# Kernel tuning notes

Measured on AMD Instinct MI355X. Metric: run time of the kernel, lower is better.

Reference implementation:

```python
import jax, jax.numpy as jnp
import numpy as np

DIM = 4096
N_HEADS = 32
N_KV_HEADS = 8
HEAD_DIM = DIM // N_HEADS  # 128
N_REP = N_HEADS // N_KV_HEADS  # 4
HIDDEN = 14336  # 4*dim -> 2/3 -> *1.3 -> round up to multiple of 256
EPS = 1e-6
BSZ, SEQLEN, CACHE_LEN = 1, 2048, 4096
ROPE_THETA = 500000.0


def setup_inputs() -> dict:
    key = jax.random.key(0)
    ks = jax.random.split(key, 16)
    s = 0.02
    x = jax.random.normal(ks[0], (BSZ, SEQLEN, DIM), jnp.float32)
    cache_k = jax.random.normal(ks[1], (BSZ, CACHE_LEN, N_KV_HEADS, HEAD_DIM), jnp.float32)
    cache_v = jax.random.normal(ks[2], (BSZ, CACHE_LEN, N_KV_HEADS, HEAD_DIM), jnp.float32)
    # causal mask over rolling cache: query i may attend to cache slot j <= (CACHE_LEN - SEQLEN) + i
    qi = jnp.arange(SEQLEN)[:, None]
    kj = jnp.arange(CACHE_LEN)[None, :]
    mask = jnp.where(kj <= (CACHE_LEN - SEQLEN) + qi, 0.0, -1e9).astype(jnp.float32)[None, None]
    # rotary freqs (cos/sin pairs) for the new seqlen positions (start of window here)
    inv = 1.0 / (ROPE_THETA ** (jnp.arange(0, HEAD_DIM, 2, dtype=jnp.float32) / HEAD_DIM))
    t = jnp.arange(SEQLEN, dtype=jnp.float32)
    ang = t[:, None] * inv[None, :]  # [S, HEAD_DIM//2]
    freqs_cis = jnp.stack([jnp.cos(ang), jnp.sin(ang)], axis=-1)  # [S, HD//2, 2]
    # params (stored as (in, out))
    wq = jax.random.normal(ks[3], (DIM, N_HEADS * HEAD_DIM), jnp.float32) * s
    wk = jax.random.normal(ks[4], (DIM, N_KV_HEADS * HEAD_DIM), jnp.float32) * s
    wv = jax.random.normal(ks[5], (DIM, N_KV_HEADS * HEAD_DIM), jnp.float32) * s
    wo = jax.random.normal(ks[6], (N_HEADS * HEAD_DIM, DIM), jnp.float32) * s
    w1 = jax.random.normal(ks[7], (DIM, HIDDEN), jnp.float32) * s
    w2 = jax.random.normal(ks[8], (HIDDEN, DIM), jnp.float32) * s
    w3 = jax.random.normal(ks[9], (DIM, HIDDEN), jnp.float32) * s
    attn_norm_w = jnp.ones((DIM,), jnp.float32)
    ffn_norm_w = jnp.ones((DIM,), jnp.float32)
    return dict(x=x, mask=mask, freqs_cis=freqs_cis, cache_k=cache_k, cache_v=cache_v,
                wq=wq, wk=wk, wv=wv, wo=wo, w1=w1, w2=w2, w3=w3,
                attn_norm_w=attn_norm_w, ffn_norm_w=ffn_norm_w)


def rmsnorm(x, w, eps=EPS):
    return x * jax.lax.rsqrt(jnp.mean(x * x, axis=-1, keepdims=True) + eps) * w


def apply_rope(xq, xk, freqs_cis):
    # xq: [B,S,Hq,D], xk: [B,S,Hkv,D]; freqs_cis: [S, D//2, 2]
    cos = freqs_cis[None, :, None, :, 0]  # [1,S,1,D//2]
    sin = freqs_cis[None, :, None, :, 1]
    def rot(t):
        tp = t.reshape(*t.shape[:-1], -1, 2)
        t0, t1 = tp[..., 0], tp[..., 1]
        o0 = t0 * cos - t1 * sin
        o1 = t0 * sin + t1 * cos
        return jnp.stack([o0, o1], axis=-1).reshape(t.shape)
    return rot(xq), rot(xk)


def reference(x, mask, freqs_cis, cache_k, cache_v, wq, wk, wv, wo, w1, w2, w3, attn_norm_w, ffn_norm_w):
    bsz, seqlen, _ = x.shape
    # --- attention norm ---
    xn = rmsnorm(x, attn_norm_w)
    # --- qkv ---
    xq = (xn @ wq).reshape(bsz, seqlen, N_HEADS, HEAD_DIM)
    xk = (xn @ wk).reshape(bsz, seqlen, N_KV_HEADS, HEAD_DIM)
    xv = (xn @ wv).reshape(bsz, seqlen, N_KV_HEADS, HEAD_DIM)
    xq, xk = apply_rope(xq, xk, freqs_cis)
    # --- rolling KV cache ---
    cache_k = jnp.concatenate([cache_k[:, seqlen:], xk], axis=1)  # [B,CL,Hkv,D]
    cache_v = jnp.concatenate([cache_v[:, seqlen:], xv], axis=1)
    keys = jnp.repeat(cache_k[:bsz], N_REP, axis=2)    # [B,CL,Hq,D]
    values = jnp.repeat(cache_v[:bsz], N_REP, axis=2)
    # --- attention ---
    scores = jnp.einsum('bqhd,bkhd->bhqk', xq, keys) / jnp.sqrt(jnp.float32(HEAD_DIM))
    scores = jax.nn.softmax(scores + mask, axis=-1)
    attn = jnp.einsum('bhqk,bkhd->bqhd', scores, values).reshape(bsz, seqlen, -1)
    h = x + attn @ wo
    # --- ffn (SwiGLU) ---
    hn = rmsnorm(h, ffn_norm_w)
    out = h + (jax.nn.silu(hn @ w1) * (hn @ w3)) @ w2
    return (out, cache_k, cache_v)
```

## Files before the change

kernel.cpp:

```cpp
#include <hip/hip_runtime.h>

typedef _Float16 h16;
typedef _Float16 h16x4 __attribute__((ext_vector_type(4)));
typedef _Float16 h16x8 __attribute__((ext_vector_type(8)));
typedef float f32x4 __attribute__((ext_vector_type(4)));
typedef unsigned short u16;

__device__ __forceinline__ f32x4 mfma16(h16x8 a, h16x8 b, f32x4 c) {
  return __builtin_amdgcn_mfma_f32_16x16x32_f16(a, b, c, 0, 0, 0);
}

typedef const __attribute__((address_space(1))) void* gas_p;
typedef __attribute__((address_space(3))) void* las_p;
__device__ __forceinline__ void ldscp16(const void* g, void* l) {
  __builtin_amdgcn_global_load_lds((gas_p)g, (las_p)l, 16, 0, 0);
}

__global__ __launch_bounds__(256) void rmsnorm_k(
    const float* __restrict__ x, const float* __restrict__ w, h16* __restrict__ out) {
  const int row = blockIdx.x, t = threadIdx.x;
  const float* xr = x + (size_t)row * 4096;
  float4 v[4];
  float ss = 0.f;
#pragma unroll
  for (int j = 0; j < 4; j++) {
    v[j] = *(const float4*)(xr + 4 * t + 1024 * j);
    ss += v[j].x * v[j].x + v[j].y * v[j].y + v[j].z * v[j].z + v[j].w * v[j].w;
  }
#pragma unroll
  for (int off = 1; off < 64; off <<= 1) ss += __shfl_xor(ss, off, 64);
  __shared__ float red[4];
  if ((t & 63) == 0) red[t >> 6] = ss;
  __syncthreads();
  float scale = rsqrtf((red[0] + red[1] + red[2] + red[3]) * (1.f / 4096.f) + 1e-6f);
  h16* orow = out + (size_t)row * 4096;
#pragma unroll
  for (int j = 0; j < 4; j++) {
    float4 wv = *(const float4*)(w + 4 * t + 1024 * j);
    h16x4 o;
    o[0] = (h16)(v[j].x * scale * wv.x);
    o[1] = (h16)(v[j].y * scale * wv.y);
    o[2] = (h16)(v[j].z * scale * wv.z);
    o[3] = (h16)(v[j].w * scale * wv.w);
    *(h16x4*)(orow + 4 * t + 1024 * j) = o;
  }
}

__global__ __launch_bounds__(256) void convw_k(
    const float* __restrict__ W, h16* __restrict__ out, int rowN, int ktiles) {
  __shared__ u16 timg[8192];
  const int t = threadIdx.x, b = blockIdx.x, kt = blockIdx.y;
  const float* src = W + (size_t)(kt * 64) * rowN + b * 128;
#pragma unroll
  for (int i = 0; i < 8; i++) {
    int c = t + (i << 8);
    int krow = c >> 5, nc = (c & 31) << 2;
    float4 v = *(const float4*)(src + (size_t)krow * rowN + nc);
    int kc = krow >> 3, e = krow & 7;
    float vals[4] = {v.x, v.y, v.z, v.w};
#pragma unroll
    for (int j = 0; j < 4; j++) {
      int m = nc + j;
      h16 hv = (h16)vals[j];
      timg[(m << 6) + ((kc ^ (m & 7)) << 3) + e] = __builtin_bit_cast(u16, hv);
    }
  }
  __syncthreads();
  uint4* dst = (uint4*)(out + ((size_t)(b * ktiles + kt) << 13));
  const uint4* s4 = (const uint4*)timg;
#pragma unroll
  for (int i = 0; i < 4; i++) dst[t + (i << 8)] = s4[t + (i << 8)];
}

template <int EPI>
__global__ __launch_bounds__(256, 2) void gemm_k(
    const h16* __restrict__ A, const h16* __restrict__ Wt,
    float* outF, h16* outH, const float* resid, const h16* uin,
    int K, int lda, int ldo, int no0) {
  __shared__ u16 sA[8192];
  __shared__ u16 sB[8192];
  const int tid = threadIdx.x, lane = tid & 63;
  const int wv = tid >> 6, wr = wv >> 1, wc = wv & 1;
  const int g = lane >> 4, lr = lane & 15;
  const int m0 = blockIdx.y << 7, n0 = blockIdx.x << 7;
  const int r8 = lane >> 3, ch = lane & 7;
  const int ktiles = K >> 6;

  f32x4 acc[4][4];
#pragma unroll
  for (int i = 0; i < 4; i++)
#pragma unroll
    for (int j = 0; j < 4; j++) acc[i][j] = {0.f, 0.f, 0.f, 0.f};

  const h16* gA = A + (size_t)(m0 + wv * 8 + r8) * lda + ((ch ^ r8) << 3);
  const h16* gB = Wt + ((size_t)blockIdx.x * ktiles << 13) + (wv << 9) + (lane << 3);
  char* lA = (char*)sA + (wv << 10);
  char* lB = (char*)sB + (wv << 10);

  for (int kt = 0; kt < ktiles; ++kt) {
    __syncthreads();
#pragma unroll
    for (int i = 0; i < 4; i++) {
      ldscp16(gA + (size_t)i * 32 * lda, lA + i * 4096);
      ldscp16(gB + i * 2048, lB + i * 4096);
    }
    gA += 64;
    gB += 8192;
    __syncthreads();
#pragma unroll
    for (int ks = 0; ks < 2; ++ks) {
      h16x8 av[4], bv[4];
#pragma unroll
      for (int f = 0; f < 4; f++) {
        int row = (wr << 6) + (f << 4) + lr;
        int cc = (ks << 2) + g;
        av[f] = *(const h16x8*)((char*)sA + row * 128 + ((cc ^ (row & 7)) << 4));
        int col = (wc << 6) + (f << 4) + lr;
        bv[f] = *(const h16x8*)((char*)sB + col * 128 + ((cc ^ (col & 7)) << 4));
      }
#pragma unroll
      for (int fi = 0; fi < 4; fi++)
#pragma unroll
        for (int fj = 0; fj < 4; fj++)
          acc[fi][fj] = mfma16(av[fi], bv[fj], acc[fi][fj]);
    }
  }
#pragma unroll
  for (int fi = 0; fi < 4; fi++) {
    const int row = m0 + (wr << 6) + (fi << 4) + (g << 2);
#pragma unroll
    for (int fj = 0; fj < 4; fj++) {
      const int col = no0 + n0 + (wc << 6) + (fj << 4) + lr;
#pragma unroll
      for (int r = 0; r < 4; r++) {
        size_t idx = (size_t)(row + r) * ldo + col;
        float vl = acc[fi][fj][r];
        if constexpr (EPI == 0) outF[idx] = vl;
        else if constexpr (EPI == 1) outH[idx] = (h16)vl;
        else if constexpr (EPI == 2) outF[idx] = resid[idx] + vl;
        else if constexpr (EPI == 3) {
          float u = (float)uin[idx];
          outH[idx] = (h16)((u / (1.f + __expf(-u))) * vl);
        } else outF[idx] = outF[idx] + vl;
      }
    }
  }
}

__global__ __launch_bounds__(256) void rope_q_k(
    const h16* __restrict__ qin, const float* __restrict__ freqs, h16* qout) {
  const int row = blockIdx.x, t = threadIdx.x;
#pragma unroll
  for (int it = 0; it < 8; ++it) {
    int pid = t + 256 * it;
    int head = pid >> 6, pp = pid & 63;
    size_t idx = (size_t)row * 4096 + head * 128 + 2 * pp;
    float x0 = (float)qin[idx], x1 = (float)qin[idx + 1];
    float cs = freqs[row * 128 + 2 * pp], sn = freqs[row * 128 + 2 * pp + 1];
    qout[idx] = (h16)(x0 * cs - x1 * sn);
    qout[idx + 1] = (h16)(x0 * sn + x1 * cs);
  }
}

__global__ __launch_bounds__(256) void cache_build_k(
    const float* __restrict__ oldK, const float* __restrict__ oldV,
    const float* __restrict__ kvraw, const float* __restrict__ freqs,
    float* __restrict__ outK, float* __restrict__ outV,
    h16* __restrict__ Kf, h16* __restrict__ Vt) {
  const int rt = blockIdx.x, kvh = blockIdx.y;
  const int r0 = rt * 64, tid = threadIdx.x;
  __shared__ u16 vtile[64][128];
#pragma unroll
  for (int it = 0; it < 16; ++it) {
    int s = tid + 256 * it;
    int rr = s >> 6, pp = s & 63;
    int r = r0 + rr;
    float k0, k1, v0, v1;
    if (r < 2048) {
      const float* kp = oldK + (size_t)(r + 2048) * 1024 + kvh * 128 + 2 * pp;
      k0 = kp[0]; k1 = kp[1];
      const float* vp = oldV + (size_t)(r + 2048) * 1024 + kvh * 128 + 2 * pp;
      v0 = vp[0]; v1 = vp[1];
    } else {
      int tpos = r - 2048;
      const float* kp = kvraw + (size_t)tpos * 2048 + kvh * 128 + 2 * pp;
      float x0 = kp[0], x1 = kp[1];
      float cs = freqs[tpos * 128 + 2 * pp], sn = freqs[tpos * 128 + 2 * pp + 1];
      k0 = x0 * cs - x1 * sn;
      k1 = x0 * sn + x1 * cs;
      const float* vp = kvraw + (size_t)tpos * 2048 + 1024 + kvh * 128 + 2 * pp;
      v0 = vp[0]; v1 = vp[1];
    }
    size_t oidx = (size_t)r * 1024 + kvh * 128 + 2 * pp;
    outK[oidx] = k0; outK[oidx + 1] = k1;
    outV[oidx] = v0; outV[oidx + 1] = v1;
    size_t kfi = (size_t)kvh * 524288 + (size_t)r * 128 + 2 * pp;
    Kf[kfi] = (h16)k0; Kf[kfi + 1] = (h16)k1;
    h16 h0 = (h16)v0, h1 = (h16)v1;
    vtile[rr][2 * pp] = __builtin_bit_cast(u16, h0);
    vtile[rr][2 * pp + 1] = __builtin_bit_cast(u16, h1);
  }
  __syncthreads();
#pragma unroll
  for (int it = 0; it < 4; ++it) {
    int c = tid + 256 * it;
    int d = c >> 3, rg = c & 7;
    u16 tmp[8];
#pragma unroll
    for (int u = 0; u < 8; u++) tmp[u] = vtile[rg * 8 + u][d];
    *(uint4*)((u16*)Vt + (size_t)kvh * 524288 + (size_t)d * 4096 + r0 + rg * 8) =
        *(uint4*)tmp;
  }
}

__global__ __launch_bounds__(256) void attn_k(
    const h16* __restrict__ Q, const h16* __restrict__ Kf,
    const h16* __restrict__ Vt, h16* __restrict__ O) {
  __shared__ u16 sK[64 * 128];
  __shared__ u16 sV[128 * 64];
  __shared__ u16 sP[4 * 16 * 64];
  const int qt = blockIdx.x, h = blockIdx.y;
  const int q0 = qt * 64, kvh = h >> 2;
  const int tid = threadIdx.x, lane = tid & 63, w = tid >> 6;
  const int g = lane >> 4, lr = lane & 15;

  h16x8 qv[4];
  {
    const h16* qp = Q + (size_t)(q0 + w * 16 + lr) * 4096 + h * 128;
#pragma unroll
    for (int ks = 0; ks < 4; ++ks) qv[ks] = *(const h16x8*)(qp + ks * 32 + g * 8);
  }
  f32x4 oacc[8];
#pragma unroll
  for (int d = 0; d < 8; ++d) oacc[d] = {0.f, 0.f, 0.f, 0.f};
  float mrow[4] = {-1e30f, -1e30f, -1e30f, -1e30f};
  float lrow[4] = {0.f, 0.f, 0.f, 0.f};

  const h16* Kb = Kf + (size_t)kvh * 524288;
  const h16* Vb = Vt + (size_t)kvh * 524288;
  const int ntiles = qt + 33;
  const float sc = 0.08838834764831845f;

  for (int jt = 0; jt < ntiles; ++jt) {
    const int j0 = jt * 64;
    __syncthreads();
#pragma unroll
    for (int i = 0; i < 4; i++) {
      int c = tid + (i << 8);
      int j = c >> 4, dc = c & 15;
      uint4 dat = *(const uint4*)(Kb + (size_t)(j0 + j) * 128 + dc * 8);
      *(uint4*)((char*)sK + j * 256 + ((dc ^ (j & 7)) << 4)) = dat;
    }
#pragma unroll
    for (int i = 0; i < 4; i++) {
      int c = tid + (i << 8);
      int d = c >> 3, jc = c & 7;
      uint4 dat = *(const uint4*)(Vb + (size_t)d * 4096 + j0 + jc * 8);
      *(uint4*)((char*)sV + d * 128 + ((jc ^ (d & 7)) << 4)) = dat;
    }
    __syncthreads();

    f32x4 sj[4];
#pragma unroll
    for (int jf = 0; jf < 4; jf++) {
      f32x4 s = {0.f, 0.f, 0.f, 0.f};
      const int j = jf * 16 + lr;
#pragma unroll
      for (int ks = 0; ks < 4; ks++) {
        const int cc = ks * 4 + g;
        h16x8 kb = *(const h16x8*)((char*)sK + j * 256 + ((cc ^ (j & 7)) << 4));
        s = mfma16(qv[ks], kb, s);
      }
      sj[jf] = s;
    }
    const bool maskt = (jt == ntiles - 1);
    float pm[4] = {-1e30f, -1e30f, -1e30f, -1e30f};
#pragma unroll
    for (int jf = 0; jf < 4; jf++)
#pragma unroll
      for (int r = 0; r < 4; r++) {
        float val = sj[jf][r] * sc;
        if (maskt) {
          int jg = j0 + jf * 16 + lr;
          int qg = q0 + w * 16 + g * 4 + r;
          if (jg > 2048 + qg) val = -1e30f;
        }
        sj[jf][r] = val;
        pm[r] = fmaxf(pm[r], val);
      }
#pragma unroll
    for (int r = 0; r < 4; r++)
#pragma unroll
      for (int off = 1; off < 16; off <<= 1)
        pm[r] = fmaxf(pm[r], __shfl_xor(pm[r], off, 16));
    float al[4], rs[4];
#pragma unroll
    for (int r = 0; r < 4; r++) {
      float mn = fmaxf(mrow[r], pm[r]);
      al[r] = __expf(mrow[r] - mn);
      mrow[r] = mn;
      rs[r] = 0.f;
    }
#pragma unroll
    for (int jf = 0; jf < 4; jf++)
#pragma unroll
      for (int r = 0; r < 4; r++) {
        float p = __expf(sj[jf][r] - mrow[r]);
        rs[r] += p;
        int qrow = g * 4 + r;
        int j = jf * 16 + lr;
        int cc = j >> 3;
        *(h16*)((char*)sP + w * 2048 + qrow * 128 + ((cc ^ (qrow & 7)) << 4) +
                (j & 7) * 2) = (h16)p;
      }
#pragma unroll
    for (int r = 0; r < 4; r++) {
#pragma unroll
      for (int off = 1; off < 16; off <<= 1) rs[r] += __shfl_xor(rs[r], off, 16);
      lrow[r] = lrow[r] * al[r] + rs[r];
    }
#pragma unroll
    for (int d = 0; d < 8; ++d)
#pragma unroll
      for (int r = 0; r < 4; r++) oacc[d][r] *= al[r];
#pragma unroll
    for (int ks = 0; ks < 2; ++ks) {
      const int cc = ks * 4 + g;
      h16x8 pa = *(const h16x8*)((char*)sP + w * 2048 + lr * 128 +
                                 ((cc ^ (lr & 7)) << 4));
#pragma unroll
      for (int df = 0; df < 8; ++df) {
        const int d = df * 16 + lr;
        h16x8 vb = *(const h16x8*)((char*)sV + d * 128 + ((cc ^ (d & 7)) << 4));
        oacc[df] = mfma16(pa, vb, oacc[df]);
      }
    }
  }
  h16* Op = O + (size_t)(q0 + w * 16 + g * 4) * 4096 + h * 128 + lr;
#pragma unroll
  for (int df = 0; df < 8; ++df)
#pragma unroll
    for (int r = 0; r < 4; r++) {
      float val = oacc[df][r] / lrow[r];
      Op[(size_t)r * 4096 + df * 16] = (h16)val;
    }
}

extern "C" void kernel_launch(void* const* d_in, const int* in_sizes, int n_in,
                              void* d_out, int out_size, void* d_ws, size_t ws_size,
                              hipStream_t stream) {
  const float* x = (const float*)d_in[0];
  const float* freqs = (const float*)d_in[2];
  const float* oldK = (const float*)d_in[3];
  const float* oldV = (const float*)d_in[4];
  const float* wq = (const float*)d_in[5];
  const float* wk = (const float*)d_in[6];
  const float* wvp = (const float*)d_in[7];
  const float* wo = (const float*)d_in[8];
  const float* w1 = (const float*)d_in[9];
  const float* w2 = (const float*)d_in[10];
  const float* w3 = (const float*)d_in[11];
  const float* anw = (const float*)d_in[12];
  const float* fnw = (const float*)d_in[13];
  float* out = (float*)d_out;
  float* outK = out + 8388608;
  float* outV = out + 12582912;

  char* ws = (char*)d_ws;
  h16* xn = (h16*)(ws + 0);
  h16* bufW = (h16*)(ws + 16777216);
  float* hbuf = (float*)(ws + 75497472);
  float* kvraw = (float*)(ws + 75497472);
  h16* kf = (h16*)(ws + 92274688);
  h16* vt = (h16*)(ws + 100663296);
  h16* ub = (h16*)(ws + 109051904);
  h16* qraw = (h16*)(ws + 109051904);
  h16* attnb = (h16*)(ws + 125829120);

  rmsnorm_k<<<2048, 256, 0, stream>>>(x, anw, xn);
  convw_k<<<dim3(32, 64), 256, 0, stream>>>(wq, bufW, 4096, 64);
  gemm_k<1><<<dim3(32, 16), 256, 0, stream>>>(xn, bufW, nullptr, qraw, nullptr,
                                              nullptr, 4096, 4096, 4096, 0);
  convw_k<<<dim3(8, 64), 256, 0, stream>>>(wk, bufW, 1024, 64);
  convw_k<<<dim3(8, 64), 256, 0, stream>>>(wvp, bufW + ((size_t)8 * 64 << 13), 1024, 64);
  gemm_k<0><<<dim3(16, 16), 256, 0, stream>>>(xn, bufW, kvraw, nullptr, nullptr,
                                              nullptr, 4096, 4096, 2048, 0);
  rope_q_k<<<2048, 256, 0, stream>>>(qraw, freqs, qraw);
  cache_build_k<<<dim3(64, 8), 256, 0, stream>>>(oldK, oldV, kvraw, freqs, outK,
                                                 outV, kf, vt);
  attn_k<<<dim3(32, 32), 256, 0, stream>>>(qraw, kf, vt, attnb);
  convw_k<<<dim3(32, 64), 256, 0, stream>>>(wo, bufW, 4096, 64);
  gemm_k<2><<<dim3(32, 16), 256, 0, stream>>>(attnb, bufW, hbuf, nullptr, x,
                                              nullptr, 4096, 4096, 4096, 0);
  rmsnorm_k<<<2048, 256, 0, stream>>>(hbuf, fnw, xn);
  convw_k<<<dim3(56, 64), 256, 0, stream>>>(w1, bufW, 14336, 64);
  gemm_k<1><<<dim3(56, 16), 256, 0, stream>>>(xn, bufW, nullptr, ub, nullptr,
                                              nullptr, 4096, 4096, 14336, 0);
  convw_k<<<dim3(56, 64), 256, 0, stream>>>(w1 + 7168, bufW, 14336, 64);
  gemm_k<1><<<dim3(56, 16), 256, 0, stream>>>(xn, bufW, nullptr, ub, nullptr,
                                              nullptr, 4096, 4096, 14336, 7168);
  convw_k<<<dim3(56, 64), 256, 0, stream>>>(w3, bufW, 14336, 64);
  gemm_k<3><<<dim3(56, 16), 256, 0, stream>>>(xn, bufW, nullptr, ub, nullptr, ub,
                                              4096, 4096, 14336, 0);
  convw_k<<<dim3(56, 64), 256, 0, stream>>>(w3 + 7168, bufW, 14336, 64);
  gemm_k<3><<<dim3(56, 16), 256, 0, stream>>>(xn, bufW, nullptr, ub, nullptr, ub,
                                              4096, 4096, 14336, 7168);
  convw_k<<<dim3(32, 112), 256, 0, stream>>>(w2, bufW, 4096, 112);
  gemm_k<2><<<dim3(32, 16), 256, 0, stream>>>(ub, bufW, out, nullptr, hbuf,
                                              nullptr, 7168, 14336, 4096, 0);
  convw_k<<<dim3(32, 112), 256, 0, stream>>>(w2 + (size_t)7168 * 4096, bufW, 4096, 112);
  gemm_k<4><<<dim3(32, 16), 256, 0, stream>>>(ub + 7168, bufW, out, nullptr,
                                              nullptr, nullptr, 7168, 14336, 4096, 0);
}
```

Before: 1.843 ms.

## Double-buffer GEMM/attention LDS loads, fuse QKV GEMM, rewrite attention with 32x32 MFMA

The GEMM kernel now double-buffers its A/B LDS tiles, so the next k-tile's async global-to-LDS copy overlaps the current tile's MFMAs, with one barrier per iteration. Q, K and V projections are fused into a single GEMM launch with a split epilogue. Attention is rewritten to use 128-query tiles, 32x32x16 MFMAs, async double-buffered K/V staging, heavy-tiles-first ordering, and a lazy rescale that only updates the running max when it grows by more than a threshold. LDS use doubles, which may cut occupancy, and the lazy-rescale softmax trades strict max tracking for fewer exp/rescale operations.

```diff
diff --git a/kernel.cpp b/kernel.cpp
--- a/kernel.cpp
+++ b/kernel.cpp
@@ -4,10 +4,14 @@
 typedef _Float16 h16x4 __attribute__((ext_vector_type(4)));
 typedef _Float16 h16x8 __attribute__((ext_vector_type(8)));
 typedef float f32x4 __attribute__((ext_vector_type(4)));
+typedef float f32x16 __attribute__((ext_vector_type(16)));
 typedef unsigned short u16;
 
 __device__ __forceinline__ f32x4 mfma16(h16x8 a, h16x8 b, f32x4 c) {
   return __builtin_amdgcn_mfma_f32_16x16x32_f16(a, b, c, 0, 0, 0);
+}
+__device__ __forceinline__ f32x16 mfma32(h16x8 a, h16x8 b, f32x16 c) {
+  return __builtin_amdgcn_mfma_f32_32x32x16_f16(a, b, c, 0, 0, 0);
 }
 
 typedef const __attribute__((address_space(1))) void* gas_p;
@@ -77,8 +81,8 @@
     const h16* __restrict__ A, const h16* __restrict__ Wt,
     float* outF, h16* outH, const float* resid, const h16* uin,
     int K, int lda, int ldo, int no0) {
-  __shared__ u16 sA[8192];
-  __shared__ u16 sB[8192];
+  __shared__ u16 sA[2][8192];
+  __shared__ u16 sB[2][8192];
   const int tid = threadIdx.x, lane = tid & 63;
   const int wv = tid >> 6, wr = wv >> 1, wc = wv & 1;
   const int g = lane >> 4, lr = lane & 15;
@@ -92,21 +96,26 @@
 #pragma unroll
     for (int j = 0; j < 4; j++) acc[i][j] = {0.f, 0.f, 0.f, 0.f};
 
-  const h16* gA = A + (size_t)(m0 + wv * 8 + r8) * lda + ((ch ^ r8) << 3);
-  const h16* gB = Wt + ((size_t)blockIdx.x * ktiles << 13) + (wv << 9) + (lane << 3);
-  char* lA = (char*)sA + (wv << 10);
-  char* lB = (char*)sB + (wv << 10);
-
+  const h16* gA0 = A + (size_t)(m0 + wv * 8 + r8) * lda + ((ch ^ r8) << 3);
+  const h16* gB0 = Wt + ((size_t)blockIdx.x * ktiles << 13) + (wv << 9) + (lane << 3);
+
+  auto stage = [&](int kt, int buf) {
+    char* lA = (char*)sA[buf] + (wv << 10);
+    char* lB = (char*)sB[buf] + (wv << 10);
+    const h16* a = gA0 + kt * 64;
+    const h16* b = gB0 + (size_t)kt * 8192;
+#pragma unroll
+    for (int i = 0; i < 4; i++) {
+      ldscp16(a + (size_t)i * 32 * lda, lA + i * 4096);
+      ldscp16(b + i * 2048, lB + i * 4096);
+    }
+  };
+
+  stage(0, 0);
+  __syncthreads();
+  int cur = 0;
   for (int kt = 0; kt < ktiles; ++kt) {
-    __syncthreads();
-#pragma unroll
-    for (int i = 0; i < 4; i++) {
-      ldscp16(gA + (size_t)i * 32 * lda, lA + i * 4096);
-      ldscp16(gB + i * 2048, lB + i * 4096);
-    }
-    gA += 64;
-    gB += 8192;
-    __syncthreads();
+    if (kt + 1 < ktiles) stage(kt + 1, cur ^ 1);
 #pragma unroll
     for (int ks = 0; ks < 2; ++ks) {
       h16x8 av[4], bv[4];
@@ -114,9 +123,9 @@
       for (int f = 0; f < 4; f++) {
         int row = (wr << 6) + (f << 4) + lr;
         int cc = (ks << 2) + g;
-        av[f] = *(const h16x8*)((char*)sA + row * 128 + ((cc ^ (row & 7)) << 4));
+        av[f] = *(const h16x8*)((char*)sA[cur] + row * 128 + ((cc ^ (row & 7)) << 4));
         int col = (wc << 6) + (f << 4) + lr;
-        bv[f] = *(const h16x8*)((char*)sB + col * 128 + ((cc ^ (col & 7)) << 4));
+        bv[f] = *(const h16x8*)((char*)sB[cur] + col * 128 + ((cc ^ (col & 7)) << 4));
       }
 #pragma unroll
       for (int fi = 0; fi < 4; fi++)
@@ -124,6 +133,8 @@
         for (int fj = 0; fj < 4; fj++)
           acc[fi][fj] = mfma16(av[fi], bv[fj], acc[fi][fj]);
     }
+    __syncthreads();
+    cur ^= 1;
   }
 #pragma unroll
   for (int fi = 0; fi < 4; fi++) {
@@ -133,15 +144,20 @@
       const int col = no0 + n0 + (wc << 6) + (fj << 4) + lr;
 #pragma unroll
       for (int r = 0; r < 4; r++) {
-        size_t idx = (size_t)(row + r) * ldo + col;
         float vl = acc[fi][fj][r];
-        if constexpr (EPI == 0) outF[idx] = vl;
-        else if constexpr (EPI == 1) outH[idx] = (h16)vl;
-        else if constexpr (EPI == 2) outF[idx] = resid[idx] + vl;
-        else if constexpr (EPI == 3) {
-          float u = (float)uin[idx];
-          outH[idx] = (h16)((u / (1.f + __expf(-u))) * vl);
-        } else outF[idx] = outF[idx] + vl;
+        if constexpr (EPI == 5) {
+          if (col < 4096) outH[(size_t)(row + r) * 4096 + col] = (h16)vl;
+          else outF[(size_t)(row + r) * 2048 + (col - 4096)] = vl;
+        } else {
+          size_t idx = (size_t)(row + r) * ldo + col;
+          if constexpr (EPI == 0) outF[idx] = vl;
+          else if constexpr (EPI == 1) outH[idx] = (h16)vl;
+          else if constexpr (EPI == 2) outF[idx] = resid[idx] + vl;
+          else if constexpr (EPI == 3) {
+            float u = (float)uin[idx];
+            outH[idx] = (h16)((u / (1.f + __expf(-u))) * vl);
+          } else outF[idx] = outF[idx] + vl;
+        }
       }
     }
   }
@@ -216,133 +232,140 @@
 __global__ __launch_bounds__(256) void attn_k(
     const h16* __restrict__ Q, const h16* __restrict__ Kf,
     const h16* __restrict__ Vt, h16* __restrict__ O) {
-  __shared__ u16 sK[64 * 128];
-  __shared__ u16 sV[128 * 64];
-  __shared__ u16 sP[4 * 16 * 64];
-  const int qt = blockIdx.x, h = blockIdx.y;
-  const int q0 = qt * 64, kvh = h >> 2;
-  const int tid = threadIdx.x, lane = tid & 63, w = tid >> 6;
-  const int g = lane >> 4, lr = lane & 15;
-
-  h16x8 qv[4];
-  {
-    const h16* qp = Q + (size_t)(q0 + w * 16 + lr) * 4096 + h * 128;
-#pragma unroll
-    for (int ks = 0; ks < 4; ++ks) qv[ks] = *(const h16x8*)(qp + ks * 32 + g * 8);
-  }
-  f32x4 oacc[8];
-#pragma unroll
-  for (int d = 0; d < 8; ++d) oacc[d] = {0.f, 0.f, 0.f, 0.f};
-  float mrow[4] = {-1e30f, -1e30f, -1e30f, -1e30f};
-  float lrow[4] = {0.f, 0.f, 0.f, 0.f};
-
+  __shared__ u16 sK[2][8192];
+  __shared__ u16 sV[2][8192];
+  __shared__ u16 sP[4][2048];
+  const int qt = 15 - blockIdx.x, h = blockIdx.y;
+  const int q0 = qt << 7, kvh = h >> 2;
+  const int tid = threadIdx.x, w = tid >> 6, lane = tid & 63;
+  const int lq = lane & 31, lh = lane >> 5;
   const h16* Kb = Kf + (size_t)kvh * 524288;
   const h16* Vb = Vt + (size_t)kvh * 524288;
-  const int ntiles = qt + 33;
+
+  h16x8 qv[8];
+  {
+    const h16* qp = Q + (size_t)(q0 + w * 32 + lq) * 4096 + h * 128 + (lh << 3);
+#pragma unroll
+    for (int c = 0; c < 8; c++) qv[c] = *(const h16x8*)(qp + c * 16);
+  }
+  f32x16 oa[4];
+#pragma unroll
+  for (int d = 0; d < 4; d++)
+#pragma unroll
+    for (int v = 0; v < 16; v++) oa[d][v] = 0.f;
+  float m2 = -3e38f, l2 = 0.f;
+  const int ntiles = 34 + 2 * qt;
   const float sc = 0.08838834764831845f;
-
-  for (int jt = 0; jt < ntiles; ++jt) {
-    const int j0 = jt * 64;
-    __syncthreads();
+  const int qg = q0 + w * 32 + lq;
+
+  auto stage = [&](int buf, int j0s) {
+    char* dK = (char*)sK[buf];
+    char* dV = (char*)sV[buf];
 #pragma unroll
     for (int i = 0; i < 4; i++) {
       int c = tid + (i << 8);
-      int j = c >> 4, dc = c & 15;
-      uint4 dat = *(const uint4*)(Kb + (size_t)(j0 + j) * 128 + dc * 8);
-      *(uint4*)((char*)sK + j * 256 + ((dc ^ (j & 7)) << 4)) = dat;
-    }
-#pragma unroll
-    for (int i = 0; i < 4; i++) {
-      int c = tid + (i << 8);
-      int d = c >> 3, jc = c & 7;
-      uint4 dat = *(const uint4*)(Vb + (size_t)d * 4096 + j0 + jc * 8);
-      *(uint4*)((char*)sV + d * 128 + ((jc ^ (d & 7)) << 4)) = dat;
+      int jl = c >> 4, kch = c & 15;
+      ldscp16(Kb + (size_t)(j0s + jl) * 128 + ((kch ^ (jl & 15)) << 3), dK + c * 16);
+      int dl = c >> 3, jch = c & 7;
+      ldscp16(Vb + (size_t)dl * 4096 + j0s + ((jch ^ (dl & 7)) << 3), dV + c * 16);
+    }
+  };
+
+  stage(0, 0);
+  __syncthreads();
+  int cur = 0;
+  for (int jt = 0; jt < ntiles; ++jt) {
+    if (jt + 1 < ntiles) stage(cur ^ 1, (jt + 1) << 6);
+    const char* bK = (const char*)sK[cur];
+    const char* bV = (const char*)sV[cur];
+    f32x16 st[2];
+#pragma unroll
+    for (int jb = 0; jb < 2; jb++) {
+      f32x16 s;
+#pragma unroll
+      for (int v = 0; v < 16; v++) s[v] = 0.f;
+      const int jr = jb * 32 + lq;
+#pragma unroll
+      for (int kc = 0; kc < 8; kc++) {
+        h16x8 ak =
+            *(const h16x8*)(bK + jr * 256 + ((((kc << 1) + lh) ^ (jr & 15)) << 4));
+        s = mfma32(ak, qv[kc], s);
+      }
+      st[jb] = s;
+    }
+    const int j0 = jt << 6;
+    const bool domask = (jt >= ntiles - 2);
+    float pm = -3e38f;
+#pragma unroll
+    for (int jb = 0; jb < 2; jb++)
+#pragma unroll
+      for (int v = 0; v < 16; v++) {
+        float val = st[jb][v] * sc;
+        if (domask) {
+          int j = j0 + jb * 32 + (v & 3) + (((v >> 2) & 3) << 3) + (lh << 2);
+          if (j > 2048 + qg) val = -1e30f;
+        }
+        st[jb][v] = val;
+        pm = fmaxf(pm, val);
+      }
+    pm = fmaxf(pm, __shfl_xor(pm, 32, 64));
+    if (__any(pm - m2 > 8.f)) {
+      float mn = fmaxf(m2, pm);
+      float al = __expf(m2 - mn);
+      m2 = mn;
+      l2 *= al;
+#pragma unroll
+      for (int d = 0; d < 4; d++) oa[d] *= al;
+    }
+    float rs = 0.f;
+#pragma unroll
+    for (int jb = 0; jb < 2; jb++)
+#pragma unroll
+      for (int v = 0; v < 16; v++) {
+        float p = __expf(st[jb][v] - m2);
+        st[jb][v] = p;
+        rs += p;
+      }
+    rs += __shfl_xor(rs, 32, 64);
+    l2 += rs;
+    char* pw = (char*)sP[w];
+#pragma unroll
+    for (int jb = 0; jb < 2; jb++)
+#pragma unroll
+      for (int b = 0; b < 4; b++) {
+        h16x4 ph;
+#pragma unroll
+        for (int i = 0; i < 4; i++) ph[i] = (h16)st[jb][(b << 2) + i];
+        *(h16x4*)(pw + lq * 128 + ((((jb << 2) + b) ^ (lq & 7)) << 4) + (lh << 3)) =
+            ph;
+      }
+    h16x8 pb[4];
+#pragma unroll
+    for (int kc = 0; kc < 4; kc++)
+      pb[kc] = *(const h16x8*)(pw + lq * 128 + ((((kc << 1) + lh) ^ (lq & 7)) << 4));
+#pragma unroll
+    for (int d = 0; d < 4; d++) {
+      const int dr = (d << 5) + lq;
+#pragma unroll
+      for (int kc = 0; kc < 4; kc++) {
+        h16x8 av =
+            *(const h16x8*)(bV + dr * 128 + ((((kc << 1) + lh) ^ (dr & 7)) << 4));
+        oa[d] = mfma32(av, pb[kc], oa[d]);
+      }
     }
     __syncthreads();
-
-    f32x4 sj[4];
-#pragma unroll
-    for (int jf = 0; jf < 4; jf++) {
-      f32x4 s = {0.f, 0.f, 0.f, 0.f};
-      const int j = jf * 16 + lr;
-#pragma unroll
-      for (int ks = 0; ks < 4; ks++) {
-        const int cc = ks * 4 + g;
-        h16x8 kb = *(const h16x8*)((char*)sK + j * 256 + ((cc ^ (j & 7)) << 4));
-        s = mfma16(qv[ks], kb, s);
-      }
-      sj[jf] = s;
-    }
-    const bool maskt = (jt == ntiles - 1);
-    float pm[4] = {-1e30f, -1e30f, -1e30f, -1e30f};
-#pragma unroll
-    for (int jf = 0; jf < 4; jf++)
-#pragma unroll
-      for (int r = 0; r < 4; r++) {
-        float val = sj[jf][r] * sc;
-        if (maskt) {
-          int jg = j0 + jf * 16 + lr;
-          int qg = q0 + w * 16 + g * 4 + r;
-          if (jg > 2048 + qg) val = -1e30f;
-        }
-        sj[jf][r] = val;
-        pm[r] = fmaxf(pm[r], val);
-      }
-#pragma unroll
-    for (int r = 0; r < 4; r++)
-#pragma unroll
-      for (int off = 1; off < 16; off <<= 1)
-        pm[r] = fmaxf(pm[r], __shfl_xor(pm[r], off, 16));
-    float al[4], rs[4];
-#pragma unroll
-    for (int r = 0; r < 4; r++) {
-      float mn = fmaxf(mrow[r], pm[r]);
-      al[r] = __expf(mrow[r] - mn);
-      mrow[r] = mn;
-      rs[r] = 0.f;
-    }
-#pragma unroll
-    for (int jf = 0; jf < 4; jf++)
-#pragma unroll
-      for (int r = 0; r < 4; r++) {
-        float p = __expf(sj[jf][r] - mrow[r]);
-        rs[r] += p;
-        int qrow = g * 4 + r;
-        int j = jf * 16 + lr;
-        int cc = j >> 3;
-        *(h16*)((char*)sP + w * 2048 + qrow * 128 + ((cc ^ (qrow & 7)) << 4) +
-                (j & 7) * 2) = (h16)p;
-      }
-#pragma unroll
-    for (int r = 0; r < 4; r++) {
-#pragma unroll
-      for (int off = 1; off < 16; off <<= 1) rs[r] += __shfl_xor(rs[r], off, 16);
-      lrow[r] = lrow[r] * al[r] + rs[r];
-    }
-#pragma unroll
-    for (int d = 0; d < 8; ++d)
-#pragma unroll
-      for (int r = 0; r < 4; r++) oacc[d][r] *= al[r];
-#pragma unroll
-    for (int ks = 0; ks < 2; ++ks) {
-      const int cc = ks * 4 + g;
-      h16x8 pa = *(const h16x8*)((char*)sP + w * 2048 + lr * 128 +
-                                 ((cc ^ (lr & 7)) << 4));
-#pragma unroll
-      for (int df = 0; df < 8; ++df) {
-        const int d = df * 16 + lr;
-        h16x8 vb = *(const h16x8*)((char*)sV + d * 128 + ((cc ^ (d & 7)) << 4));
-        oacc[df] = mfma16(pa, vb, oacc[df]);
-      }
-    }
-  }
-  h16* Op = O + (size_t)(q0 + w * 16 + g * 4) * 4096 + h * 128 + lr;
-#pragma unroll
-  for (int df = 0; df < 8; ++df)
-#pragma unroll
-    for (int r = 0; r < 4; r++) {
-      float val = oacc[df][r] / lrow[r];
-      Op[(size_t)r * 4096 + df * 16] = (h16)val;
+    cur ^= 1;
+  }
+  float rl = 1.f / l2;
+  h16* Op = O + (size_t)qg * 4096 + h * 128;
+#pragma unroll
+  for (int d = 0; d < 4; d++)
+#pragma unroll
+    for (int b = 0; b < 4; b++) {
+      h16x4 ov;
+#pragma unroll
+      for (int i = 0; i < 4; i++) ov[i] = (h16)(oa[d][(b << 2) + i] * rl);
+      *(h16x4*)(Op + (d << 5) + (b << 3) + (lh << 2)) = ov;
     }
 }
 
@@ -379,16 +402,14 @@
 
   rmsnorm_k<<<2048, 256, 0, stream>>>(x, anw, xn);
   convw_k<<<dim3(32, 64), 256, 0, stream>>>(wq, bufW, 4096, 64);
-  gemm_k<1><<<dim3(32, 16), 256, 0, stream>>>(xn, bufW, nullptr, qraw, nullptr,
-                                              nullptr, 4096, 4096, 4096, 0);
-  convw_k<<<dim3(8, 64), 256, 0, stream>>>(wk, bufW, 1024, 64);
-  convw_k<<<dim3(8, 64), 256, 0, stream>>>(wvp, bufW + ((size_t)8 * 64 << 13), 1024, 64);
-  gemm_k<0><<<dim3(16, 16), 256, 0, stream>>>(xn, bufW, kvraw, nullptr, nullptr,
-                                              nullptr, 4096, 4096, 2048, 0);
+  convw_k<<<dim3(8, 64), 256, 0, stream>>>(wk, bufW + ((size_t)32 * 64 << 13), 1024, 64);
+  convw_k<<<dim3(8, 64), 256, 0, stream>>>(wvp, bufW + ((size_t)40 * 64 << 13), 1024, 64);
+  gemm_k<5><<<dim3(48, 16), 256, 0, stream>>>(xn, bufW, kvraw, qraw, nullptr,
+                                              nullptr, 4096, 4096, 0, 0);
   rope_q_k<<<2048, 256, 0, stream>>>(qraw, freqs, qraw);
   cache_build_k<<<dim3(64, 8), 256, 0, stream>>>(oldK, oldV, kvraw, freqs, outK,
                                                  outV, kf, vt);
-  attn_k<<<dim3(32, 32), 256, 0, stream>>>(qraw, kf, vt, attnb);
+  attn_k<<<dim3(16, 32), 256, 0, stream>>>(qraw, kf, vt, attnb);
   convw_k<<<dim3(32, 64), 256, 0, stream>>>(wo, bufW, 4096, 64);
   gemm_k<2><<<dim3(32, 16), 256, 0, stream>>>(attnb, bufW, hbuf, nullptr, x,
                                               nullptr, 4096, 4096, 4096, 0);
```

New measurement: 1.833 ms. No clear change (-0.5%).
